# Kernel tuning notes

Hardware: AMD Instinct MI355X
Metric: run time of the kernel (lower is better)

Reference implementation:

```python
import jax, jax.numpy as jnp
import numpy as np
import math


def setup_inputs() -> dict:
    key = jax.random.key(0)
    k_x, k_q, k_k, k_v, k_o = jax.random.split(key, 5)
    B, S, D_IN, H, D_K, D_V, D_OUT = 1, 4096, 512, 8, 64, 64, 512
    # torch.rand -> uniform[0,1); scaled by 0.02 to keep softmax unsaturated
    scale = 0.02
    return {
        "x": jax.random.normal(k_x, (B, S, D_IN), dtype=jnp.float32),
        "W_q": jax.random.uniform(k_q, (H, D_IN, D_K), dtype=jnp.float32) * scale,
        "W_k": jax.random.uniform(k_k, (H, D_IN, D_K), dtype=jnp.float32) * scale,
        "W_v": jax.random.uniform(k_v, (H, D_IN, D_V), dtype=jnp.float32) * scale,
        "W_o": jax.random.uniform(k_o, (H, D_V, D_OUT), dtype=jnp.float32) * scale,
    }


def reference(x, W_q, W_k, W_v, W_o):
    # x: [B,S,d_in]; W_q/W_k: [H,d_in,d_k]; W_v: [H,d_in,d_v]; W_o: [H,d_v,d_out]
    S = x.shape[-2]
    d_key = W_k.shape[-1]
    Q = jnp.einsum('hjk,blj->bhlk', W_q, x)   # [B,H,S,d_k]
    K = jnp.einsum('hjk,blj->bhlk', W_k, x)   # [B,H,S,d_k]
    V = jnp.einsum('hjk,blj->bhlk', W_v, x)   # [B,H,S,d_v]
    # causal mask: True where masked (strict upper triangle)
    mask = jnp.triu(jnp.ones((S, S), dtype=bool), k=1)  # [S,S]
    scores = jnp.einsum('bhik,bhjk->bhij', Q, K)        # [B,H,S,S]
    scores = jnp.where(mask, -jnp.inf, scores)
    # is_scaled=True: divide by sqrt(d_key) before softmax
    weights = jax.nn.softmax(scores / math.sqrt(d_key), axis=-1)
    weights = jnp.where(mask, 0.0, weights)
    values = jnp.einsum('bhij,bhjv->bhiv', weights, V)  # [B,H,S,d_v]
    return jnp.einsum('hvk,bhlv->blk', W_o, values)     # [B,S,d_out]
```

## Files before the change

### kernel.cpp

```cpp
#include <hip/hip_runtime.h>
#include <hip/hip_bf16.h>
#include <math.h>

#define S_LEN 4096
#define NH    8

typedef __attribute__((ext_vector_type(8))) short bf16x8;
typedef __attribute__((ext_vector_type(4))) short bf16x4;
typedef __attribute__((ext_vector_type(4))) float f32x4;
typedef __attribute__((ext_vector_type(16))) float f32x16;

#define QSCALE 0.18033688011112042f

#define WAIT_VM4 0x0F74
#define WAIT_VM0 0x0F70

__device__ __forceinline__ short f2bf(float f) {
    union { float f; unsigned u; } v; v.f = f;
    unsigned r = v.u + 0x7fffu + ((v.u >> 16) & 1u);
    return (short)(r >> 16);
}

__device__ __forceinline__ int pk2(float a, float b) {
    __hip_bfloat162 t = __float22bfloat162_rn(make_float2(a, b));
    union { __hip_bfloat162 h; int i; } u; u.h = t;
    return u.i;
}

__device__ __forceinline__ void gload16(const void* g, void* l) {
    __builtin_amdgcn_global_load_lds(
        (const __attribute__((address_space(1))) unsigned*)g,
        (__attribute__((address_space(3))) unsigned*)l, 16, 0, 0);
}

__device__ __forceinline__ void stage_tile(const short* gsrc, size_t gstride,
                                           short* tile, int t)
{
    const int wave = t >> 6, lane = t & 63;
    const int sub = lane >> 3;
    const int cg  = (lane & 7) ^ sub;
#pragma unroll
    for (int j = 0; j < 2; ++j) {
        const int chunk = wave * 2 + j;
        const int row = chunk * 8 + sub;
        gload16(gsrc + (size_t)row * gstride + cg * 8, tile + chunk * 512);
    }
}

__device__ __forceinline__ bf16x8 frag(const short* tile, int row, int cg) {
    return *(const bf16x8*)&tile[row * 64 + ((cg ^ (row & 7)) << 3)];
}

__device__ __forceinline__ void gemm_mainloop_512(
    const short* __restrict__ Arow, const short* __restrict__ Brow,
    short* As, short* Bs, f32x4 acc[4], int t)
{
    const int wave = t >> 6, lane = t & 63, n16 = lane & 15, quad = lane >> 4;
    stage_tile(Arow, 512, As, t);
    stage_tile(Brow, 512, Bs, t);
    for (int c = 0; c < 8; ++c) {
        const int cur = c & 1;
        __builtin_amdgcn_s_barrier();
        if (c < 7) {
            stage_tile(Arow + (c + 1) * 64, 512, As + (1 - cur) * 4096, t);
            stage_tile(Brow + (c + 1) * 64, 512, Bs + (1 - cur) * 4096, t);
            __builtin_amdgcn_s_waitcnt(WAIT_VM4);
        } else {
            __builtin_amdgcn_s_waitcnt(WAIT_VM0);
        }
        __builtin_amdgcn_s_barrier();
        const short* as = As + cur * 4096;
        const short* bs = Bs + cur * 4096;
#pragma unroll
        for (int kh = 0; kh < 2; ++kh) {
            const bf16x8 a = frag(as, wave * 16 + n16, kh * 4 + quad);
#pragma unroll
            for (int nt = 0; nt < 4; ++nt) {
                const bf16x8 b = frag(bs, nt * 16 + n16, kh * 4 + quad);
                acc[nt] = __builtin_amdgcn_mfma_f32_16x16x32_bf16(a, b, acc[nt], 0, 0, 0);
            }
        }
    }
}

__global__ __launch_bounds__(256) void prep_kernel(
    const float* __restrict__ x,
    const float* __restrict__ Wq, const float* __restrict__ Wk,
    const float* __restrict__ Wv, const float* __restrict__ Wo,
    short* __restrict__ xb, short* __restrict__ Wqkvt, short* __restrict__ Wot)
{
    __shared__ short T[64 * 66];
    const int b = blockIdx.x, t = threadIdx.x;
    if (b < 1024) {
        const size_t idx = (size_t)b * 2048 + t * 8;
        const float4 a = *(const float4*)&x[idx];
        const float4 c = *(const float4*)&x[idx + 4];
        bf16x8 o;
        o[0] = f2bf(a.x); o[1] = f2bf(a.y); o[2] = f2bf(a.z); o[3] = f2bf(a.w);
        o[4] = f2bf(c.x); o[5] = f2bf(c.y); o[6] = f2bf(c.z); o[7] = f2bf(c.w);
        *(bf16x8*)&xb[idx] = o;
        return;
    }
    const int c4 = (t & 15) * 4, rsub = t >> 4;
    const int orow = t >> 2, oc16 = (t & 3) * 16;
    if (b < 1216) {
        const int jj = b - 1024, g = jj >> 3, kb = jj & 7;
        const int which = g >> 3, h = g & 7;
        const float* W = ((which == 0) ? Wq : (which == 1) ? Wk : Wv) + (size_t)h * 512 * 64;
#pragma unroll
        for (int p = 0; p < 4; ++p) {
            const int row = p * 16 + rsub;
            const float4 v = *(const float4*)&W[(size_t)(kb * 64 + row) * 64 + c4];
            T[(c4 + 0) * 66 + row] = f2bf(v.x);
            T[(c4 + 1) * 66 + row] = f2bf(v.y);
            T[(c4 + 2) * 66 + row] = f2bf(v.z);
            T[(c4 + 3) * 66 + row] = f2bf(v.w);
        }
        __syncthreads();
        short* O = &Wqkvt[((size_t)g * 64 + orow) * 512 + kb * 64];
        *(bf16x8*)&O[oc16]     = *(const bf16x8*)&T[orow * 66 + oc16];
        *(bf16x8*)&O[oc16 + 8] = *(const bf16x8*)&T[orow * 66 + oc16 + 8];
    } else {
        const int jj = b - 1216, h = jj >> 3, nb = jj & 7;
        const float* W = Wo + (size_t)h * 64 * 512;
#pragma unroll
        for (int p = 0; p < 4; ++p) {
            const int row = p * 16 + rsub;
            const float4 v = *(const float4*)&W[(size_t)row * 512 + nb * 64 + c4];
            T[(c4 + 0) * 66 + row] = f2bf(v.x);
            T[(c4 + 1) * 66 + row] = f2bf(v.y);
            T[(c4 + 2) * 66 + row] = f2bf(v.z);
            T[(c4 + 3) * 66 + row] = f2bf(v.w);
        }
        __syncthreads();
        short* O = &Wot[((size_t)nb * 64 + orow) * 512 + h * 64];
        *(bf16x8*)&O[oc16]     = *(const bf16x8*)&T[orow * 66 + oc16];
        *(bf16x8*)&O[oc16 + 8] = *(const bf16x8*)&T[orow * 66 + oc16 + 8];
    }
}

__global__ __launch_bounds__(256) void qkv_gemm_kernel(
    const short* __restrict__ xb, const short* __restrict__ Wqkvt,
    short* __restrict__ Qg, short* __restrict__ Kg, short* __restrict__ Vtg)
{
    __shared__ short smem[16384];
    short* As = smem;
    short* Bs = smem + 8192;
    const int sblk = blockIdx.x, g = blockIdx.y;
    const int which = g >> 3, h = g & 7;
    const int t = threadIdx.x;
    const int wave = t >> 6, lane = t & 63, n16 = lane & 15, quad = lane >> 4;

    f32x4 acc[4] = {{0,0,0,0},{0,0,0,0},{0,0,0,0},{0,0,0,0}};
    gemm_mainloop_512(xb + (size_t)sblk * 64 * 512, Wqkvt + (size_t)g * 64 * 512,
                      As, Bs, acc, t);

    if (which < 2) {
        const float scale = (which == 0) ? QSCALE : 1.0f;
        short* O = ((which == 0) ? Qg : Kg) + (size_t)h * S_LEN * 64;
#pragma unroll
        for (int nt = 0; nt < 4; ++nt)
#pragma unroll
            for (int r = 0; r < 4; ++r) {
                const int s = sblk * 64 + wave * 16 + quad * 4 + r;
                O[(size_t)s * 64 + nt * 16 + n16] = f2bf(acc[nt][r] * scale);
            }
    } else {
        __syncthreads();
        short* Tr = smem;
#pragma unroll
        for (int nt = 0; nt < 4; ++nt)
#pragma unroll
            for (int r = 0; r < 4; ++r)
                Tr[(nt * 16 + n16) * 66 + wave * 16 + quad * 4 + r] = f2bf(acc[nt][r]);
        __syncthreads();
        short* O = Vtg + (size_t)h * 64 * S_LEN + sblk * 64;
        const int r4 = t >> 2, c16 = (t & 3) * 16;
        *(bf16x8*)&O[(size_t)r4 * S_LEN + c16]     = *(const bf16x8*)&Tr[r4 * 66 + c16];
        *(bf16x8*)&O[(size_t)r4 * S_LEN + c16 + 8] = *(const bf16x8*)&Tr[r4 * 66 + c16 + 8];
    }
}

__global__ __launch_bounds__(256) void out_gemm_kernel(
    const short* __restrict__ vals, const short* __restrict__ Wot, float* __restrict__ out)
{
    __shared__ short smem[16384];
    short* As = smem;
    short* Bs = smem + 8192;
    const int sblk = blockIdx.x, g = blockIdx.y;
    const int t = threadIdx.x;
    const int wave = t >> 6, lane = t & 63, n16 = lane & 15, quad = lane >> 4;

    f32x4 acc[4] = {{0,0,0,0},{0,0,0,0},{0,0,0,0},{0,0,0,0}};
    gemm_mainloop_512(vals + (size_t)sblk * 64 * 512, Wot + (size_t)g * 64 * 512,
                      As, Bs, acc, t);

#pragma unroll
    for (int nt = 0; nt < 4; ++nt)
#pragma unroll
        for (int r = 0; r < 4; ++r) {
            const int s = sblk * 64 + wave * 16 + quad * 4 + r;
            out[(size_t)s * 512 + g * 64 + nt * 16 + n16] = acc[nt][r];
        }
}

__global__ __launch_bounds__(256, 3) void attn_kernel(
    const short* __restrict__ Qg, const short* __restrict__ Kg,
    const short* __restrict__ Vtg, float* __restrict__ Opart, float* __restrict__ Lpart)
{
    __shared__ short Ks[2][4096];
    __shared__ short Vs[2][4096];
    __shared__ short Ps[4 * 32 * 72];

    const int id = blockIdx.x;
    const int h  = id & 7;
    const int c  = 79 - (id >> 3);
    int qs, j;
    if (c < 8)       { qs = c;                   j = 0; }
    else if (c < 24) { qs = 8 + ((c - 8) >> 1);  j = (c - 8) & 1; }
    else if (c < 48) { qs = 16 + (c - 24) / 3;   j = (c - 24) % 3; }
    else             { qs = 24 + ((c - 48) >> 2); j = (c - 48) & 3; }
    const int k0   = j * 16;
    const int kend = min(k0 + 16, 2 * qs + 2);

    const short* Kh  = Kg  + (size_t)h * S_LEN * 64;
    const short* Vth = Vtg + (size_t)h * 64 * S_LEN;

    const int t = threadIdx.x;
    const int wave = t >> 6, lane = t & 63, l31 = lane & 31, half = lane >> 5;
    const int qg = qs * 128 + wave * 32 + l31;

    const short* Qr = Qg + (size_t)h * S_LEN * 64 + (size_t)qg * 64;
    bf16x8 bq[4];
#pragma unroll
    for (int kc = 0; kc < 4; ++kc)
        bq[kc] = *(const bf16x8*)&Qr[kc * 16 + half * 8];

    bf16x8 ones;
#pragma unroll
    for (int i = 0; i < 8; ++i) ones[i] = (short)0x3F80;

    f32x16 z16;
#pragma unroll
    for (int r = 0; r < 16; ++r) z16[r] = 0.f;

    f32x16 oacc[2], lacc;
#pragma unroll
    for (int r = 0; r < 16; ++r) { oacc[0][r] = 0.f; oacc[1][r] = 0.f; lacc[r] = 0.f; }
    short* Pw = Ps + wave * (32 * 72);

    stage_tile(Kh + (size_t)k0 * 64 * 64, 64, Ks[0], t);
    stage_tile(Vth + k0 * 64, S_LEN, Vs[0], t);

    for (int kb = k0; kb < kend; ++kb) {
        const int cur = (kb - k0) & 1;
        __builtin_amdgcn_s_barrier();
        if (kb + 1 < kend) {
            stage_tile(Kh + (size_t)(kb + 1) * 64 * 64, 64, Ks[1 - cur], t);
            stage_tile(Vth + (kb + 1) * 64, S_LEN, Vs[1 - cur], t);
            __builtin_amdgcn_s_waitcnt(WAIT_VM4);
        } else {
            __builtin_amdgcn_s_waitcnt(WAIT_VM0);
        }
        __builtin_amdgcn_s_barrier();

        f32x16 sc0, sc1;
        {
            const bf16x8 a0 = frag(Ks[cur], l31,      half);
            const bf16x8 a1 = frag(Ks[cur], 32 + l31, half);
            sc0 = __builtin_amdgcn_mfma_f32_32x32x16_bf16(a0, bq[0], z16, 0, 0, 0);
            sc1 = __builtin_amdgcn_mfma_f32_32x32x16_bf16(a1, bq[0], z16, 0, 0, 0);
        }
#pragma unroll
        for (int kc = 1; kc < 4; ++kc) {
            const bf16x8 a0 = frag(Ks[cur], l31,      kc * 2 + half);
            const bf16x8 a1 = frag(Ks[cur], 32 + l31, kc * 2 + half);
            sc0 = __builtin_amdgcn_mfma_f32_32x32x16_bf16(a0, bq[kc], sc0, 0, 0, 0);
            sc1 = __builtin_amdgcn_mfma_f32_32x32x16_bf16(a1, bq[kc], sc1, 0, 0, 0);
        }

        if (kb * 64 + 63 > qg) {
#pragma unroll
            for (int r = 0; r < 16; ++r) {
                const int keyb = kb * 64 + (r & 3) + 8 * (r >> 2) + 4 * half;
                if (keyb > qg)      sc0[r] = -1e30f;
                if (keyb + 32 > qg) sc1[r] = -1e30f;
            }
        }

#pragma unroll
        for (int g2 = 0; g2 < 4; ++g2) {
            int2 w;
            w.x = pk2(__builtin_amdgcn_exp2f(sc0[4 * g2 + 0]),
                      __builtin_amdgcn_exp2f(sc0[4 * g2 + 1]));
            w.y = pk2(__builtin_amdgcn_exp2f(sc0[4 * g2 + 2]),
                      __builtin_amdgcn_exp2f(sc0[4 * g2 + 3]));
            *(int2*)&Pw[l31 * 72 + g2 * 8 + half * 4] = w;
            int2 w2;
            w2.x = pk2(__builtin_amdgcn_exp2f(sc1[4 * g2 + 0]),
                       __builtin_amdgcn_exp2f(sc1[4 * g2 + 1]));
            w2.y = pk2(__builtin_amdgcn_exp2f(sc1[4 * g2 + 2]),
                       __builtin_amdgcn_exp2f(sc1[4 * g2 + 3]));
            *(int2*)&Pw[l31 * 72 + 32 + g2 * 8 + half * 4] = w2;
        }
        __builtin_amdgcn_wave_barrier();

#pragma unroll
        for (int kc = 0; kc < 4; ++kc) {
            const bf16x8 bp = *(const bf16x8*)&Pw[l31 * 72 + kc * 16 + half * 8];
            const bf16x8 a0 = frag(Vs[cur], l31,      kc * 2 + half);
            const bf16x8 a1 = frag(Vs[cur], 32 + l31, kc * 2 + half);
            oacc[0] = __builtin_amdgcn_mfma_f32_32x32x16_bf16(a0, bp, oacc[0], 0, 0, 0);
            oacc[1] = __builtin_amdgcn_mfma_f32_32x32x16_bf16(a1, bp, oacc[1], 0, 0, 0);
            lacc    = __builtin_amdgcn_mfma_f32_32x32x16_bf16(ones, bp, lacc, 0, 0, 0);
        }
        __builtin_amdgcn_wave_barrier();
    }

    float* tileO = Opart + (size_t)(h * 80 + c) * (64 * 128);
    float* tileL = Lpart + (h * 80 + c) * 128;
    if (half == 0) tileL[wave * 32 + l31] = lacc[0];
#pragma unroll
    for (int mt = 0; mt < 2; ++mt)
#pragma unroll
        for (int r = 0; r < 16; ++r) {
            const int v = mt * 32 + (r & 3) + 8 * (r >> 2) + 4 * half;
            tileO[(v << 7) + wave * 32 + l31] = (mt ? oacc[1][r] : oacc[0][r]);
        }
}

__global__ __launch_bounds__(256) void combine_norm_kernel(
    const float* __restrict__ Opart, const float* __restrict__ Lpart,
    short* __restrict__ vals)
{
    __shared__ short T[128 * 66];
    const int id = blockIdx.x;
    const int h = id & 7, qs = id >> 3;
    int c0, nj;
    if (qs < 8)       { c0 = qs;                 nj = 1; }
    else if (qs < 16) { c0 = 8 + 2 * (qs - 8);   nj = 2; }
    else if (qs < 24) { c0 = 24 + 3 * (qs - 16); nj = 3; }
    else              { c0 = 48 + 4 * (qs - 24); nj = 4; }
    const int base = h * 80 + c0;

    const int t = threadIdx.x;
    const int q0 = (t & 31) * 4;
    const int vr = t >> 5;

    f32x4 L = {0, 0, 0, 0};
    for (int j = 0; j < nj; ++j)
        L += *(const f32x4*)&Lpart[(base + j) * 128 + q0];
    const f32x4 inv = {1.f / L[0], 1.f / L[1], 1.f / L[2], 1.f / L[3]};

#pragma unroll
    for (int pass = 0; pass < 8; ++pass) {
        const int v = vr + pass * 8;
        f32x4 s = {0, 0, 0, 0};
        for (int j = 0; j < nj; ++j)
            s += *(const f32x4*)&Opart[(size_t)(base + j) * 8192 + (v << 7) + q0];
        T[(q0 + 0) * 66 + v] = f2bf(s[0] * inv[0]);
        T[(q0 + 1) * 66 + v] = f2bf(s[1] * inv[1]);
        T[(q0 + 2) * 66 + v] = f2bf(s[2] * inv[2]);
        T[(q0 + 3) * 66 + v] = f2bf(s[3] * inv[3]);
    }
    __syncthreads();
    const int q = t >> 1, vh = (t & 1) * 32;
    const size_t row = (size_t)(qs * 128 + q) * 512 + h * 64 + vh;
#pragma unroll
    for (int u = 0; u < 4; ++u)
        *(bf16x8*)&vals[row + u * 8] = *(const bf16x8*)&T[q * 66 + vh + u * 8];
}

extern "C" void kernel_launch(void* const* d_in, const int* in_sizes, int n_in,
                              void* d_out, int out_size, void* d_ws, size_t ws_size,
                              hipStream_t stream)
{
    const float* x  = (const float*)d_in[0];
    const float* Wq = (const float*)d_in[1];
    const float* Wk = (const float*)d_in[2];
    const float* Wv = (const float*)d_in[3];
    const float* Wo = (const float*)d_in[4];
    float* out = (float*)d_out;

    short* xb    = (short*)d_ws;
    short* Wqkvt = xb + 2097152;
    short* Wot   = Wqkvt + 786432;
    short* Qg    = Wot + 262144;
    short* Kg    = Qg + 2097152;
    short* Vtg   = Kg + 2097152;
    short* vals  = Vtg + 2097152;
    float* Opart = (float*)(vals + 2097152);
    float* Lpart = Opart + (size_t)640 * 8192;

    prep_kernel<<<1280, 256, 0, stream>>>(x, Wq, Wk, Wv, Wo, xb, Wqkvt, Wot);
    qkv_gemm_kernel<<<dim3(64, 24), 256, 0, stream>>>(xb, Wqkvt, Qg, Kg, Vtg);
    attn_kernel<<<640, 256, 0, stream>>>(Qg, Kg, Vtg, Opart, Lpart);
    combine_norm_kernel<<<256, 256, 0, stream>>>(Opart, Lpart, vals);
    out_gemm_kernel<<<dim3(64, 8), 256, 0, stream>>>(vals, Wot, out);
}
```

Measured before the change: 135.2 us.

## Keep softmax probabilities in registers via permlane swap; widen QKV GEMM tiles

The attention kernel no longer writes exp'd scores to LDS and reads them back as MFMA operands. It builds the bf16 B-operand in registers using permlane32_swap. The row-sum is now a per-lane scalar add plus a cross-half shuffle, replacing the extra ones-MFMA per k-chunk. Separately, the QKV GEMM now processes 128 rows per block, so each B tile is reused twice and the grid is halved. This adds register pressure and relies on permlane32_swap being available on the target.

Measured after the change: 135.2 us. About the same (+0.1%).

```diff
diff --git a/kernel.cpp b/kernel.cpp
--- a/kernel.cpp
+++ b/kernel.cpp
@@ -9,9 +9,11 @@
 typedef __attribute__((ext_vector_type(4))) short bf16x4;
 typedef __attribute__((ext_vector_type(4))) float f32x4;
 typedef __attribute__((ext_vector_type(16))) float f32x16;
+typedef __attribute__((ext_vector_type(2)))  int   int32x2;
 
 #define QSCALE 0.18033688011112042f
 
+#define WAIT_VM6 0x0F76
 #define WAIT_VM4 0x0F74
 #define WAIT_VM0 0x0F70
 
@@ -49,6 +51,26 @@
 
 __device__ __forceinline__ bf16x8 frag(const short* tile, int row, int cg) {
     return *(const bf16x8*)&tile[row * 64 + ((cg ^ (row & 7)) << 3)];
+}
+
+__device__ __forceinline__ bf16x8 mk_bp(const f32x16& sc, const int p, float& lsum)
+{
+    const float e0 = __builtin_amdgcn_exp2f(sc[8 * p + 0]);
+    const float e1 = __builtin_amdgcn_exp2f(sc[8 * p + 1]);
+    const float e2 = __builtin_amdgcn_exp2f(sc[8 * p + 2]);
+    const float e3 = __builtin_amdgcn_exp2f(sc[8 * p + 3]);
+    const float e4 = __builtin_amdgcn_exp2f(sc[8 * p + 4]);
+    const float e5 = __builtin_amdgcn_exp2f(sc[8 * p + 5]);
+    const float e6 = __builtin_amdgcn_exp2f(sc[8 * p + 6]);
+    const float e7 = __builtin_amdgcn_exp2f(sc[8 * p + 7]);
+    lsum += ((e0 + e1) + (e2 + e3)) + ((e4 + e5) + (e6 + e7));
+    int we0 = pk2(e0, e1), we1 = pk2(e2, e3);
+    int wo0 = pk2(e4, e5), wo1 = pk2(e6, e7);
+    const int32x2 r0 = __builtin_amdgcn_permlane32_swap(we0, wo0, false, false);
+    const int32x2 r1 = __builtin_amdgcn_permlane32_swap(we1, wo1, false, false);
+    union { int i[4]; bf16x8 v; } u;
+    u.i[0] = r0[0]; u.i[1] = r1[0]; u.i[2] = r0[1]; u.i[3] = r1[1];
+    return u.v;
 }
 
 __device__ __forceinline__ void gemm_mainloop_512(
@@ -143,41 +165,82 @@
     const short* __restrict__ xb, const short* __restrict__ Wqkvt,
     short* __restrict__ Qg, short* __restrict__ Kg, short* __restrict__ Vtg)
 {
-    __shared__ short smem[16384];
+    __shared__ short smem[24576];
     short* As = smem;
-    short* Bs = smem + 8192;
+    short* Bs = smem + 16384;
     const int sblk = blockIdx.x, g = blockIdx.y;
     const int which = g >> 3, h = g & 7;
     const int t = threadIdx.x;
     const int wave = t >> 6, lane = t & 63, n16 = lane & 15, quad = lane >> 4;
 
-    f32x4 acc[4] = {{0,0,0,0},{0,0,0,0},{0,0,0,0},{0,0,0,0}};
-    gemm_mainloop_512(xb + (size_t)sblk * 64 * 512, Wqkvt + (size_t)g * 64 * 512,
-                      As, Bs, acc, t);
+    const short* Arow = xb + (size_t)sblk * 128 * 512;
+    const short* Brow = Wqkvt + (size_t)g * 64 * 512;
+
+    f32x4 acc[2][4] = {{{0,0,0,0},{0,0,0,0},{0,0,0,0},{0,0,0,0}},
+                       {{0,0,0,0},{0,0,0,0},{0,0,0,0},{0,0,0,0}}};
+
+    stage_tile(Arow,            512, As,        t);
+    stage_tile(Arow + 64 * 512, 512, As + 4096, t);
+    stage_tile(Brow,            512, Bs,        t);
+    for (int c = 0; c < 8; ++c) {
+        const int cur = c & 1;
+        __builtin_amdgcn_s_barrier();
+        if (c < 7) {
+            stage_tile(Arow + (c + 1) * 64,            512, As + (1 - cur) * 8192,        t);
+            stage_tile(Arow + 64 * 512 + (c + 1) * 64, 512, As + (1 - cur) * 8192 + 4096, t);
+            stage_tile(Brow + (c + 1) * 64,            512, Bs + (1 - cur) * 4096,        t);
+            __builtin_amdgcn_s_waitcnt(WAIT_VM6);
+        } else {
+            __builtin_amdgcn_s_waitcnt(WAIT_VM0);
+        }
+        __builtin_amdgcn_s_barrier();
+        const short* as = As + cur * 8192;
+        const short* bs = Bs + cur * 4096;
+        const int r0 = wave * 32 + n16;
+        const short* a_sub = as + (r0 >> 6) * 4096;
+#pragma unroll
+        for (int kh = 0; kh < 2; ++kh) {
+            const bf16x8 a0 = frag(a_sub, r0 & 63,        kh * 4 + quad);
+            const bf16x8 a1 = frag(a_sub, (r0 & 63) + 16, kh * 4 + quad);
+#pragma unroll
+            for (int nt = 0; nt < 4; ++nt) {
+                const bf16x8 b = frag(bs, nt * 16 + n16, kh * 4 + quad);
+                acc[0][nt] = __builtin_amdgcn_mfma_f32_16x16x32_bf16(a0, b, acc[0][nt], 0, 0, 0);
+                acc[1][nt] = __builtin_amdgcn_mfma_f32_16x16x32_bf16(a1, b, acc[1][nt], 0, 0, 0);
+            }
+        }
+    }
 
     if (which < 2) {
         const float scale = (which == 0) ? QSCALE : 1.0f;
         short* O = ((which == 0) ? Qg : Kg) + (size_t)h * S_LEN * 64;
 #pragma unroll
-        for (int nt = 0; nt < 4; ++nt)
-#pragma unroll
-            for (int r = 0; r < 4; ++r) {
-                const int s = sblk * 64 + wave * 16 + quad * 4 + r;
-                O[(size_t)s * 64 + nt * 16 + n16] = f2bf(acc[nt][r] * scale);
-            }
+        for (int m = 0; m < 2; ++m)
+#pragma unroll
+            for (int nt = 0; nt < 4; ++nt)
+#pragma unroll
+                for (int r = 0; r < 4; ++r) {
+                    const int s = sblk * 128 + wave * 32 + m * 16 + quad * 4 + r;
+                    O[(size_t)s * 64 + nt * 16 + n16] = f2bf(acc[m][nt][r] * scale);
+                }
     } else {
         __syncthreads();
         short* Tr = smem;
 #pragma unroll
-        for (int nt = 0; nt < 4; ++nt)
-#pragma unroll
-            for (int r = 0; r < 4; ++r)
-                Tr[(nt * 16 + n16) * 66 + wave * 16 + quad * 4 + r] = f2bf(acc[nt][r]);
+        for (int m = 0; m < 2; ++m)
+#pragma unroll
+            for (int nt = 0; nt < 4; ++nt)
+#pragma unroll
+                for (int r = 0; r < 4; ++r)
+                    Tr[(nt * 16 + n16) * 130 + wave * 32 + m * 16 + quad * 4 + r] =
+                        f2bf(acc[m][nt][r]);
         __syncthreads();
-        short* O = Vtg + (size_t)h * 64 * S_LEN + sblk * 64;
-        const int r4 = t >> 2, c16 = (t & 3) * 16;
-        *(bf16x8*)&O[(size_t)r4 * S_LEN + c16]     = *(const bf16x8*)&Tr[r4 * 66 + c16];
-        *(bf16x8*)&O[(size_t)r4 * S_LEN + c16 + 8] = *(const bf16x8*)&Tr[r4 * 66 + c16 + 8];
+        short* O = Vtg + (size_t)h * 64 * S_LEN + sblk * 128;
+        const int vr = t >> 2, c32 = (t & 3) * 32;
+#pragma unroll
+        for (int u = 0; u < 4; ++u)
+            *(bf16x8*)&O[(size_t)vr * S_LEN + c32 + u * 8] =
+                *(const bf16x8*)&Tr[vr * 130 + c32 + u * 8];
     }
 }
 
@@ -210,7 +273,6 @@
 {
     __shared__ short Ks[2][4096];
     __shared__ short Vs[2][4096];
-    __shared__ short Ps[4 * 32 * 72];
 
     const int id = blockIdx.x;
     const int h  = id & 7;
@@ -236,18 +298,14 @@
     for (int kc = 0; kc < 4; ++kc)
         bq[kc] = *(const bf16x8*)&Qr[kc * 16 + half * 8];
 
-    bf16x8 ones;
-#pragma unroll
-    for (int i = 0; i < 8; ++i) ones[i] = (short)0x3F80;
-
     f32x16 z16;
 #pragma unroll
     for (int r = 0; r < 16; ++r) z16[r] = 0.f;
 
-    f32x16 oacc[2], lacc;
-#pragma unroll
-    for (int r = 0; r < 16; ++r) { oacc[0][r] = 0.f; oacc[1][r] = 0.f; lacc[r] = 0.f; }
-    short* Pw = Ps + wave * (32 * 72);
+    f32x16 oacc[2];
+#pragma unroll
+    for (int r = 0; r < 16; ++r) { oacc[0][r] = 0.f; oacc[1][r] = 0.f; }
+    float llane = 0.f;
 
     stage_tile(Kh + (size_t)k0 * 64 * 64, 64, Ks[0], t);
     stage_tile(Vth + k0 * 64, S_LEN, Vs[0], t);
@@ -288,38 +346,25 @@
             }
         }
 
-#pragma unroll
-        for (int g2 = 0; g2 < 4; ++g2) {
-            int2 w;
-            w.x = pk2(__builtin_amdgcn_exp2f(sc0[4 * g2 + 0]),
-                      __builtin_amdgcn_exp2f(sc0[4 * g2 + 1]));
-            w.y = pk2(__builtin_amdgcn_exp2f(sc0[4 * g2 + 2]),
-                      __builtin_amdgcn_exp2f(sc0[4 * g2 + 3]));
-            *(int2*)&Pw[l31 * 72 + g2 * 8 + half * 4] = w;
-            int2 w2;
-            w2.x = pk2(__builtin_amdgcn_exp2f(sc1[4 * g2 + 0]),
-                       __builtin_amdgcn_exp2f(sc1[4 * g2 + 1]));
-            w2.y = pk2(__builtin_amdgcn_exp2f(sc1[4 * g2 + 2]),
-                       __builtin_amdgcn_exp2f(sc1[4 * g2 + 3]));
-            *(int2*)&Pw[l31 * 72 + 32 + g2 * 8 + half * 4] = w2;
-        }
-        __builtin_amdgcn_wave_barrier();
+        bf16x8 bp[4];
+        bp[0] = mk_bp(sc0, 0, llane);
+        bp[1] = mk_bp(sc0, 1, llane);
+        bp[2] = mk_bp(sc1, 0, llane);
+        bp[3] = mk_bp(sc1, 1, llane);
 
 #pragma unroll
         for (int kc = 0; kc < 4; ++kc) {
-            const bf16x8 bp = *(const bf16x8*)&Pw[l31 * 72 + kc * 16 + half * 8];
             const bf16x8 a0 = frag(Vs[cur], l31,      kc * 2 + half);
             const bf16x8 a1 = frag(Vs[cur], 32 + l31, kc * 2 + half);
-            oacc[0] = __builtin_amdgcn_mfma_f32_32x32x16_bf16(a0, bp, oacc[0], 0, 0, 0);
-            oacc[1] = __builtin_amdgcn_mfma_f32_32x32x16_bf16(a1, bp, oacc[1], 0, 0, 0);
-            lacc    = __builtin_amdgcn_mfma_f32_32x32x16_bf16(ones, bp, lacc, 0, 0, 0);
-        }
-        __builtin_amdgcn_wave_barrier();
+            oacc[0] = __builtin_amdgcn_mfma_f32_32x32x16_bf16(a0, bp[kc], oacc[0], 0, 0, 0);
+            oacc[1] = __builtin_amdgcn_mfma_f32_32x32x16_bf16(a1, bp[kc], oacc[1], 0, 0, 0);
+        }
     }
 
     float* tileO = Opart + (size_t)(h * 80 + c) * (64 * 128);
     float* tileL = Lpart + (h * 80 + c) * 128;
-    if (half == 0) tileL[wave * 32 + l31] = lacc[0];
+    const float lq = llane + __shfl_xor(llane, 32, 64);
+    if (half == 0) tileL[wave * 32 + l31] = lq;
 #pragma unroll
     for (int mt = 0; mt < 2; ++mt)
 #pragma unroll
@@ -393,7 +438,7 @@
     float* Lpart = Opart + (size_t)640 * 8192;
 
     prep_kernel<<<1280, 256, 0, stream>>>(x, Wq, Wk, Wv, Wo, xb, Wqkvt, Wot);
-    qkv_gemm_kernel<<<dim3(64, 24), 256, 0, stream>>>(xb, Wqkvt, Qg, Kg, Vtg);
+    qkv_gemm_kernel<<<dim3(32, 24), 256, 0, stream>>>(xb, Wqkvt, Qg, Kg, Vtg);
     attn_kernel<<<640, 256, 0, stream>>>(Qg, Kg, Vtg, Opart, Lpart);
     combine_norm_kernel<<<256, 256, 0, stream>>>(Opart, Lpart, vals);
     out_gemm_kernel<<<dim3(64, 8), 256, 0, stream>>>(vals, Wot, out);
```
